# Kernel tuning notes

Hardware: AMD Instinct MI355X
Metric: run time of the kernel (lower is better)

The kernel has to match this reference:

```python
import jax, jax.numpy as jnp
import numpy as np

MAX_ACF_LAG = 6
TOP_K_FFT = 3
CLIP_VALUE = 5.0
EPS = 1e-8


def setup_inputs() -> dict:
    key = jax.random.key(0)
    x = jax.random.normal(key, (128, 4096, 32), dtype=jnp.float32)
    return {"x": x}


def _per_var_features(x):
    # x: [B, T, V] -> [B, V, 10 + MAX_ACF_LAG]
    B, T, V = x.shape
    mean = jnp.mean(x, axis=1)                      # [B, V]
    xc = x - mean[:, None, :]                       # centered, [B, T, V]
    var = jnp.mean(xc * xc, axis=1)                 # [B, V]
    std = jnp.sqrt(var + EPS)
    z = xc / std[:, None, :]
    skew = jnp.mean(z ** 3, axis=1)
    kurt = jnp.mean(z ** 4, axis=1)
    mn = jnp.min(x, axis=1)
    mx = jnp.max(x, axis=1)
    # linear trend slope via least squares on t = 0..T-1
    t = jnp.arange(T, dtype=x.dtype)
    tc = t - jnp.mean(t)
    slope = jnp.einsum('btv,t->bv', xc, tc) / jnp.sum(tc * tc)
    # top-k FFT magnitudes (exclude DC), normalized by T
    mag = jnp.abs(jnp.fft.rfft(x, axis=1))[:, 1:, :] / T   # [B, F, V]
    topk, _ = jax.lax.top_k(jnp.transpose(mag, (0, 2, 1)), TOP_K_FFT)  # [B, V, k]
    # autocorrelation at lags 1..MAX_ACF_LAG
    denom = jnp.sum(xc * xc, axis=1) + EPS          # [B, V]
    acfs = [jnp.sum(xc[:, :-lag, :] * xc[:, lag:, :], axis=1) / denom
            for lag in range(1, MAX_ACF_LAG + 1)]
    acf = jnp.stack(acfs, axis=-1)                  # [B, V, L]
    base = jnp.stack([mean, std, skew, kurt, mn, mx, slope], axis=-1)  # [B, V, 7]
    return jnp.concatenate([base, topk, acf], axis=-1)  # [B, V, 16]


def reference(x):
    feats = _per_var_features(x)                    # [B, V, 16]
    f_mean = jnp.mean(feats, axis=1)                # [B, 16]
    f_std = jnp.std(feats, axis=1)                  # [B, 16]
    out = jnp.concatenate([f_mean, f_std], axis=-1) # [B, 32]
    return jnp.clip(out, -CLIP_VALUE, CLIP_VALUE)
```

## Files before the change

### kernel.cpp

```cpp
#include <hip/hip_runtime.h>
#include <math.h>

#define T_LEN 4096
#define M_LEN 2048
#define V_DIM 32
#define B_DIM 128
#define NTHREADS 512
#define NWAVES (NTHREADS / 64)

__device__ __forceinline__ int SW(int i) { return i ^ (((i >> 4) & 7) << 1); }

__device__ __forceinline__ int fpos(int k) {
    return ((k & 3) << 9) | (((k >> 2) & 3) << 7) | (((k >> 4) & 3) << 5)
         | (((k >> 6) & 3) << 3) | (((k >> 8) & 3) << 1) | ((k >> 10) & 1);
}

__device__ __forceinline__ void ins3(float& a0, float& a1, float& a2, float m) {
    if (m > a0) { a2 = a1; a1 = a0; a0 = m; }
    else if (m > a1) { a2 = a1; a1 = m; }
    else if (m > a2) { a2 = m; }
}

template <typename Op>
__device__ __forceinline__ void block_reduce2(float& a, float& b, float* scr, Op op) {
    #pragma unroll
    for (int o = 32; o > 0; o >>= 1) {
        a = op(a, __shfl_down(a, o));
        b = op(b, __shfl_down(b, o));
    }
    int lane = threadIdx.x & 63, w = threadIdx.x >> 6;
    if (lane == 0) { scr[w * 2] = a; scr[w * 2 + 1] = b; }
    __syncthreads();
    if (threadIdx.x == 0) {
        float ra = scr[0], rb = scr[1];
        #pragma unroll
        for (int i = 1; i < NWAVES; i++) { ra = op(ra, scr[i * 2]); rb = op(rb, scr[i * 2 + 1]); }
        scr[2 * NWAVES] = ra; scr[2 * NWAVES + 1] = rb;
    }
    __syncthreads();
    a = scr[2 * NWAVES]; b = scr[2 * NWAVES + 1];
    __syncthreads();
}

__device__ __forceinline__ void block_reduce_sum10(float* v, float* scr) {
    #pragma unroll
    for (int r = 0; r < 10; r++) {
        #pragma unroll
        for (int o = 32; o > 0; o >>= 1) v[r] += __shfl_down(v[r], o);
    }
    int lane = threadIdx.x & 63, w = threadIdx.x >> 6;
    if (lane == 0) {
        #pragma unroll
        for (int r = 0; r < 10; r++) scr[w * 10 + r] = v[r];
    }
    __syncthreads();
    if (threadIdx.x < 10) {
        float s = 0.f;
        #pragma unroll
        for (int i = 0; i < NWAVES; i++) s += scr[i * 10 + threadIdx.x];
        scr[NWAVES * 10 + threadIdx.x] = s;
    }
    __syncthreads();
    #pragma unroll
    for (int r = 0; r < 10; r++) v[r] = scr[NWAVES * 10 + r];
    __syncthreads();
}

__global__ __launch_bounds__(NTHREADS, 8)
void ts_feat_kernel(const float* __restrict__ x, float* __restrict__ feats) {
    __shared__ __align__(16) float data[2][T_LEN];
    __shared__ float scr[128];
    float* const fd = &data[0][0];
    float2* const Z = reinterpret_cast<float2*>(fd);

    const int tid = threadIdx.x;
    const int bid  = blockIdx.x;
    const int xcd  = bid & 7;
    const int idx  = bid >> 3;
    const int b    = xcd + ((idx >> 4) << 3);
    const int pair = idx & 15;
    const int v0   = pair * 2;
    const int sid0 = b * V_DIM + v0;

    const float2* __restrict__ p2 =
        reinterpret_cast<const float2*>(x + (size_t)b * T_LEN * V_DIM + v0);

    float s0 = 0.f, s1 = 0.f;
    float mn0 = 3.4e38f, mn1 = 3.4e38f, mx0 = -3.4e38f, mx1 = -3.4e38f;
    const int comp = tid & 1;
    #pragma unroll
    for (int i = 0; i < T_LEN / NTHREADS; i++) {
        int t = tid + i * NTHREADS;
        float2 val = p2[(size_t)t * (V_DIM / 2)];
        int f = SW(t >> 1);
        fd[(f << 1) + comp] = val.x;
        fd[T_LEN + (f << 1) + comp] = val.y;
        s0 += val.x; s1 += val.y;
        mn0 = fminf(mn0, val.x); mn1 = fminf(mn1, val.y);
        mx0 = fmaxf(mx0, val.x); mx1 = fmaxf(mx1, val.y);
    }
    __syncthreads();
    block_reduce2(s0, s1, scr, [](float a, float c) { return a + c; });
    block_reduce2(mn0, mn1, scr, [](float a, float c) { return fminf(a, c); });
    block_reduce2(mx0, mx1, scr, [](float a, float c) { return fmaxf(a, c); });

    const float mean0 = s0 * (1.f / T_LEN);
    const float mean1 = s1 * (1.f / T_LEN);

    #pragma unroll 1
    for (int si = 0; si < 2; si++) {
        const float m = si ? mean1 : mean0;
        const int fb = (si << 11) + (tid << 2);
        float4 q0 = *reinterpret_cast<const float4*>(&Z[SW(fb)]);
        float4 q1 = *reinterpret_cast<const float4*>(&Z[SW(fb + 2)]);
        float4 q2 = make_float4(0.f, 0.f, 0.f, 0.f);
        float2 q3 = make_float2(0.f, 0.f);
        const bool interior = (tid < NTHREADS - 1);
        if (interior) {
            q2 = *reinterpret_cast<const float4*>(&Z[SW(fb + 4)]);
            q3 = Z[SW(fb + 6)];
        }
        float xc[8] = {q0.x - m, q0.y - m, q0.z - m, q0.w - m,
                       q1.x - m, q1.y - m, q1.z - m, q1.w - m};
        float xb[6];
        if (interior) {
            xb[0] = q2.x - m; xb[1] = q2.y - m; xb[2] = q2.z - m;
            xb[3] = q2.w - m; xb[4] = q3.x - m; xb[5] = q3.y - m;
        } else {
            #pragma unroll
            for (int u = 0; u < 6; u++) xb[u] = 0.f;
        }
        float acc[10];
        #pragma unroll
        for (int r = 0; r < 10; r++) acc[r] = 0.f;
        const float tf0 = (float)(tid * 8) - 2047.5f;
        #pragma unroll
        for (int u = 0; u < 8; u++) {
            float c = xc[u], c2v = c * c;
            acc[0] += c2v;
            acc[1] += c2v * c;
            acc[2] += c2v * c2v;
            acc[3] += c * (tf0 + (float)u);
        }
        #pragma unroll
        for (int L = 1; L <= 6; L++) {
            #pragma unroll
            for (int u = 0; u < 8; u++) {
                float nx = (u + L < 8) ? xc[u + L] : xb[u + L - 8];
                acc[3 + L] += xc[u] * nx;
            }
        }
        block_reduce_sum10(acc, scr);

        if (tid == 0) {
            const float c2 = acc[0], c3 = acc[1], c4 = acc[2], ct = acc[3];
            float var = c2 * (1.f / T_LEN);
            float sd  = sqrtf(var + 1e-8f);
            float i3  = 1.f / (sd * sd * sd);
            float skew = c3 * (1.f / T_LEN) * i3;
            float kurt = c4 * (1.f / T_LEN) * i3 / sd;
            float slope = ct / 5726622720.f;
            float dn = c2 + 1e-8f;
            float* fp = feats + (size_t)(sid0 + si) * 16;
            fp[0] = m; fp[1] = sd; fp[2] = skew; fp[3] = kurt;
            fp[4] = si ? mn1 : mn0;
            fp[5] = si ? mx1 : mx0;
            fp[6] = slope;
            fp[10] = acc[4] / dn;
            fp[11] = acc[5] / dn;
            fp[12] = acc[6] / dn;
            fp[13] = acc[7] / dn;
            fp[14] = acc[8] / dn;
            fp[15] = acc[9] / dn;
        }
    }

    #pragma unroll
    for (int st = 0; st < 5; st++) {
        const int lq = 9 - 2 * st;
        const int q  = 1 << lq;
        const float scale = -3.06796158e-3f * (float)(1 << (2 * st));
        __syncthreads();
        #pragma unroll
        for (int si = 0; si < 2; si++) {
            const int w = tid;
            const int g = w >> lq;
            const int j = w & (q - 1);
            const int base = (si << 11) + (g << (lq + 2)) + j;
            const int p0 = SW(base), p1 = SW(base + q);
            const int p2i = SW(base + 2 * q), p3 = SW(base + 3 * q);
            float2 a = Z[p0], bb = Z[p1], c = Z[p2i], d = Z[p3];
            float t0r = a.x + c.x,  t0i = a.y + c.y;
            float t1r = a.x - c.x,  t1i = a.y - c.y;
            float t2r = bb.x + d.x, t2i = bb.y + d.y;
            float t3r = bb.x - d.x, t3i = bb.y - d.y;
            float sn, cs;
            __sincosf(scale * (float)j, &sn, &cs);
            float c2 = cs * cs - sn * sn, s2 = 2.f * cs * sn;
            float c3 = c2 * cs - s2 * sn, s3 = c2 * sn + s2 * cs;
            float y1r = t1r + t3i, y1i = t1i - t3r;
            float y2r = t0r - t2r, y2i = t0i - t2i;
            float y3r = t1r - t3i, y3i = t1i + t3r;
            Z[p0]  = make_float2(t0r + t2r, t0i + t2i);
            Z[p1]  = make_float2(y1r * cs - y1i * sn, y1r * sn + y1i * cs);
            Z[p2i] = make_float2(y2r * c2 - y2i * s2, y2r * s2 + y2i * c2);
            Z[p3]  = make_float2(y3r * c3 - y3i * s3, y3r * s3 + y3i * c3);
        }
    }
    __syncthreads();
    #pragma unroll
    for (int bfI = 0; bfI < 4; bfI++) {
        int mI = tid + (bfI << 9);
        int si = mI >> 10, g = mI & 1023;
        int p = SW((si << 11) + (g << 1));
        float4 ab = *reinterpret_cast<float4*>(&Z[p]);
        float4 o;
        o.x = ab.x + ab.z; o.y = ab.y + ab.w;
        o.z = ab.x - ab.z; o.w = ab.y - ab.w;
        *reinterpret_cast<float4*>(&Z[p]) = o;
    }
    __syncthreads();

    const float inv_T = 1.f / (float)T_LEN;
    #pragma unroll 1
    for (int si = 0; si < 2; si++) {
        const int zb = si << 11;
        float a0 = -1.f, a1 = -1.f, a2 = -1.f;
        #pragma unroll
        for (int i = 0; i < M_LEN / NTHREADS; i++) {
            int k  = 1 + tid + i * NTHREADS;
            int ka = k & (M_LEN - 1);
            int kb = (M_LEN - k) & (M_LEN - 1);
            float2 Za = Z[zb + SW(fpos(ka))];
            float2 Zb = Z[zb + SW(fpos(kb))];
            float Er = 0.5f * (Za.x + Zb.x);
            float Ei = 0.5f * (Za.y - Zb.y);
            float Or = 0.5f * (Za.y + Zb.y);
            float Oi = 0.5f * (Zb.x - Za.x);
            float ang = (float)k * (-3.14159265358979f / (float)M_LEN);
            float sn, cs; __sincosf(ang, &sn, &cs);
            float Xr = Er + cs * Or - sn * Oi;
            float Xi = Ei + cs * Oi + sn * Or;
            float mag = sqrtf(Xr * Xr + Xi * Xi);
            ins3(a0, a1, a2, mag);
        }
        #pragma unroll
        for (int o = 32; o > 0; o >>= 1) {
            float b0 = __shfl_down(a0, o), b1 = __shfl_down(a1, o), b2 = __shfl_down(a2, o);
            ins3(a0, a1, a2, b0); ins3(a0, a1, a2, b1); ins3(a0, a1, a2, b2);
        }
        int lane = tid & 63, w = tid >> 6;
        if (lane == 0) { scr[w * 3 + 0] = a0; scr[w * 3 + 1] = a1; scr[w * 3 + 2] = a2; }
        __syncthreads();
        if (tid == 0) {
            float t0 = scr[0], t1 = scr[1], t2 = scr[2];
            #pragma unroll
            for (int w2 = 1; w2 < NWAVES; w2++) {
                ins3(t0, t1, t2, scr[w2 * 3 + 0]);
                ins3(t0, t1, t2, scr[w2 * 3 + 1]);
                ins3(t0, t1, t2, scr[w2 * 3 + 2]);
            }
            float* fp = feats + (size_t)(sid0 + si) * 16;
            fp[7] = t0 * inv_T; fp[8] = t1 * inv_T; fp[9] = t2 * inv_T;
        }
        __syncthreads();
    }
}

__global__ void ts_reduce_kernel(const float* __restrict__ feats, float* __restrict__ out) {
    int tg = blockIdx.x * blockDim.x + threadIdx.x;
    if (tg >= B_DIM * 16) return;
    int b = tg >> 4, f = tg & 15;
    const float* fp = feats + (size_t)b * V_DIM * 16 + f;
    float vals[V_DIM];
    float s = 0.f;
    #pragma unroll
    for (int v = 0; v < V_DIM; v++) { vals[v] = fp[v * 16]; s += vals[v]; }
    float m = s * (1.f / V_DIM);
    float q = 0.f;
    #pragma unroll
    for (int v = 0; v < V_DIM; v++) { float d = vals[v] - m; q += d * d; }
    float sd = sqrtf(q * (1.f / V_DIM));
    out[(size_t)b * 32 + f]      = fminf(fmaxf(m,  -5.f), 5.f);
    out[(size_t)b * 32 + 16 + f] = fminf(fmaxf(sd, -5.f), 5.f);
}

extern "C" void kernel_launch(void* const* d_in, const int* in_sizes, int n_in,
                              void* d_out, int out_size, void* d_ws, size_t ws_size,
                              hipStream_t stream) {
    const float* x = (const float*)d_in[0];
    float* out = (float*)d_out;
    float* feats = (float*)d_ws;

    hipLaunchKernelGGL(ts_feat_kernel, dim3(B_DIM * V_DIM / 2), dim3(NTHREADS), 0, stream,
                       x, feats);
    hipLaunchKernelGGL(ts_reduce_kernel, dim3(8), dim3(256), 0, stream,
                       feats, out);
}
```

Baseline: 155.0 us.

## Cut block barriers by merging reductions and overlapping stats with FFT stages

The three separate block reductions (sum, min, max) are merged into one pass with a single pair of barriers. The per-series 10-value moment/ACF reduction now writes partials for both series at once and finishes in the shadow of the first FFT stage, and feature finalisation overlaps the second stage. The final radix-2 pass is folded into the post-processing reads, and the top-3 search handles both series in one loop. The ACF now uses a sliding window over preceding elements rather than following ones. All of this removes many __syncthreads and one LDS round trip, at the cost of more shared scratch and registers.

```diff
diff --git a/kernel.cpp b/kernel.cpp
--- a/kernel.cpp
+++ b/kernel.cpp
@@ -6,7 +6,7 @@
 #define V_DIM 32
 #define B_DIM 128
 #define NTHREADS 512
-#define NWAVES (NTHREADS / 64)
+#define NWAVES 8
 
 __device__ __forceinline__ int SW(int i) { return i ^ (((i >> 4) & 7) << 1); }
 
@@ -21,55 +21,55 @@
     else if (m > a2) { a2 = m; }
 }
 
-template <typename Op>
-__device__ __forceinline__ void block_reduce2(float& a, float& b, float* scr, Op op) {
-    #pragma unroll
-    for (int o = 32; o > 0; o >>= 1) {
-        a = op(a, __shfl_down(a, o));
-        b = op(b, __shfl_down(b, o));
-    }
-    int lane = threadIdx.x & 63, w = threadIdx.x >> 6;
-    if (lane == 0) { scr[w * 2] = a; scr[w * 2 + 1] = b; }
-    __syncthreads();
-    if (threadIdx.x == 0) {
-        float ra = scr[0], rb = scr[1];
-        #pragma unroll
-        for (int i = 1; i < NWAVES; i++) { ra = op(ra, scr[i * 2]); rb = op(rb, scr[i * 2 + 1]); }
-        scr[2 * NWAVES] = ra; scr[2 * NWAVES + 1] = rb;
-    }
-    __syncthreads();
-    a = scr[2 * NWAVES]; b = scr[2 * NWAVES + 1];
-    __syncthreads();
-}
-
-__device__ __forceinline__ void block_reduce_sum10(float* v, float* scr) {
-    #pragma unroll
-    for (int r = 0; r < 10; r++) {
-        #pragma unroll
-        for (int o = 32; o > 0; o >>= 1) v[r] += __shfl_down(v[r], o);
-    }
-    int lane = threadIdx.x & 63, w = threadIdx.x >> 6;
-    if (lane == 0) {
-        #pragma unroll
-        for (int r = 0; r < 10; r++) scr[w * 10 + r] = v[r];
-    }
-    __syncthreads();
-    if (threadIdx.x < 10) {
-        float s = 0.f;
-        #pragma unroll
-        for (int i = 0; i < NWAVES; i++) s += scr[i * 10 + threadIdx.x];
-        scr[NWAVES * 10 + threadIdx.x] = s;
-    }
-    __syncthreads();
-    #pragma unroll
-    for (int r = 0; r < 10; r++) v[r] = scr[NWAVES * 10 + r];
-    __syncthreads();
+#define SCR_A_PART 0
+#define SCR_A_FIN  48
+#define SCR_B_PART 64
+#define SCR_B_FIN  704
+#define SCR_C_PART 724
+#define SCR_SIZE   772
+
+template <int ST>
+__device__ __forceinline__ void fft_stage(float2* Z, int tid) {
+    constexpr int lq = 9 - 2 * ST;
+    constexpr int q  = 1 << lq;
+    const float scale = -3.06796158e-3f * (float)(1 << (2 * ST));
+    #pragma unroll
+    for (int si = 0; si < 2; si++) {
+        const int g = tid >> lq;
+        const int j = tid & (q - 1);
+        const int base = (si << 11) + (g << (lq + 2)) + j;
+        const int p0 = SW(base), p1 = SW(base + q);
+        const int p2i = SW(base + 2 * q), p3 = SW(base + 3 * q);
+        float2 a = Z[p0], bb = Z[p1], c = Z[p2i], d = Z[p3];
+        float t0r = a.x + c.x,  t0i = a.y + c.y;
+        float t1r = a.x - c.x,  t1i = a.y - c.y;
+        float t2r = bb.x + d.x, t2i = bb.y + d.y;
+        float t3r = bb.x - d.x, t3i = bb.y - d.y;
+        float sn, cs;
+        __sincosf(scale * (float)j, &sn, &cs);
+        float c2 = cs * cs - sn * sn, s2 = 2.f * cs * sn;
+        float c3 = c2 * cs - s2 * sn, s3 = c2 * sn + s2 * cs;
+        float y1r = t1r + t3i, y1i = t1i - t3r;
+        float y2r = t0r - t2r, y2i = t0i - t2i;
+        float y3r = t1r - t3i, y3i = t1i + t3r;
+        Z[p0]  = make_float2(t0r + t2r, t0i + t2i);
+        Z[p1]  = make_float2(y1r * cs - y1i * sn, y1r * sn + y1i * cs);
+        Z[p2i] = make_float2(y2r * c2 - y2i * s2, y2r * s2 + y2i * c2);
+        Z[p3]  = make_float2(y3r * c3 - y3i * s3, y3r * s3 + y3i * c3);
+    }
+}
+
+__device__ __forceinline__ float2 rdpost(const float2* Z, int zb, int p) {
+    int e = p & ~1;
+    float4 v = *reinterpret_cast<const float4*>(&Z[zb + SW(e)]);
+    return (p & 1) ? make_float2(v.x - v.z, v.y - v.w)
+                   : make_float2(v.x + v.z, v.y + v.w);
 }
 
 __global__ __launch_bounds__(NTHREADS, 8)
 void ts_feat_kernel(const float* __restrict__ x, float* __restrict__ feats) {
     __shared__ __align__(16) float data[2][T_LEN];
-    __shared__ float scr[128];
+    __shared__ float scr[SCR_SIZE];
     float* const fd = &data[0][0];
     float2* const Z = reinterpret_cast<float2*>(fd);
 
@@ -89,7 +89,7 @@
     float mn0 = 3.4e38f, mn1 = 3.4e38f, mx0 = -3.4e38f, mx1 = -3.4e38f;
     const int comp = tid & 1;
     #pragma unroll
-    for (int i = 0; i < T_LEN / NTHREADS; i++) {
+    for (int i = 0; i < 8; i++) {
         int t = tid + i * NTHREADS;
         float2 val = p2[(size_t)t * (V_DIM / 2)];
         int f = SW(t >> 1);
@@ -99,13 +99,32 @@
         mn0 = fminf(mn0, val.x); mn1 = fminf(mn1, val.y);
         mx0 = fmaxf(mx0, val.x); mx1 = fmaxf(mx1, val.y);
     }
-    __syncthreads();
-    block_reduce2(s0, s1, scr, [](float a, float c) { return a + c; });
-    block_reduce2(mn0, mn1, scr, [](float a, float c) { return fminf(a, c); });
-    block_reduce2(mx0, mx1, scr, [](float a, float c) { return fmaxf(a, c); });
-
-    const float mean0 = s0 * (1.f / T_LEN);
-    const float mean1 = s1 * (1.f / T_LEN);
+    #pragma unroll
+    for (int o = 32; o > 0; o >>= 1) {
+        s0 += __shfl_down(s0, o); s1 += __shfl_down(s1, o);
+        mn0 = fminf(mn0, __shfl_down(mn0, o)); mn1 = fminf(mn1, __shfl_down(mn1, o));
+        mx0 = fmaxf(mx0, __shfl_down(mx0, o)); mx1 = fmaxf(mx1, __shfl_down(mx1, o));
+    }
+    const int lane = tid & 63, wv = tid >> 6;
+    if (lane == 0) {
+        float* p = &scr[SCR_A_PART + wv * 6];
+        p[0] = s0; p[1] = s1; p[2] = mn0; p[3] = mn1; p[4] = mx0; p[5] = mx1;
+    }
+    __syncthreads();
+    if (tid < 6) {
+        float r = scr[SCR_A_PART + tid];
+        #pragma unroll
+        for (int w = 1; w < NWAVES; w++) {
+            float v = scr[SCR_A_PART + w * 6 + tid];
+            r = (tid < 2) ? (r + v) : ((tid < 4) ? fminf(r, v) : fmaxf(r, v));
+        }
+        scr[SCR_A_FIN + tid] = r;
+    }
+    __syncthreads();
+    const float mean0 = scr[SCR_A_FIN + 0] * (1.f / T_LEN);
+    const float mean1 = scr[SCR_A_FIN + 1] * (1.f / T_LEN);
+    float fmn = 0.f, fmx = 0.f;
+    if (tid < 2) { fmn = scr[SCR_A_FIN + 2 + tid]; fmx = scr[SCR_A_FIN + 4 + tid]; }
 
     #pragma unroll 1
     for (int si = 0; si < 2; si++) {
@@ -113,157 +132,137 @@
         const int fb = (si << 11) + (tid << 2);
         float4 q0 = *reinterpret_cast<const float4*>(&Z[SW(fb)]);
         float4 q1 = *reinterpret_cast<const float4*>(&Z[SW(fb + 2)]);
-        float4 q2 = make_float4(0.f, 0.f, 0.f, 0.f);
-        float2 q3 = make_float2(0.f, 0.f);
-        const bool interior = (tid < NTHREADS - 1);
-        if (interior) {
-            q2 = *reinterpret_cast<const float4*>(&Z[SW(fb + 4)]);
-            q3 = Z[SW(fb + 6)];
-        }
-        float xc[8] = {q0.x - m, q0.y - m, q0.z - m, q0.w - m,
-                       q1.x - m, q1.y - m, q1.z - m, q1.w - m};
-        float xb[6];
-        if (interior) {
-            xb[0] = q2.x - m; xb[1] = q2.y - m; xb[2] = q2.z - m;
-            xb[3] = q2.w - m; xb[4] = q3.x - m; xb[5] = q3.y - m;
-        } else {
-            #pragma unroll
-            for (int u = 0; u < 6; u++) xb[u] = 0.f;
+        float p1v = 0.f, p2v = 0.f, p3v = 0.f, p4v = 0.f, p5v = 0.f, p6v = 0.f;
+        if (tid > 0) {
+            float2 tv = Z[SW(fb - 3)];
+            float4 tq = *reinterpret_cast<const float4*>(&Z[SW(fb - 2)]);
+            p6v = tv.x - m; p5v = tv.y - m;
+            p4v = tq.x - m; p3v = tq.y - m; p2v = tq.z - m; p1v = tq.w - m;
         }
         float acc[10];
         #pragma unroll
         for (int r = 0; r < 10; r++) acc[r] = 0.f;
         const float tf0 = (float)(tid * 8) - 2047.5f;
+        float xs[8] = {q0.x, q0.y, q0.z, q0.w, q1.x, q1.y, q1.z, q1.w};
         #pragma unroll
         for (int u = 0; u < 8; u++) {
-            float c = xc[u], c2v = c * c;
+            float c = xs[u] - m;
+            float c2v = c * c;
             acc[0] += c2v;
             acc[1] += c2v * c;
             acc[2] += c2v * c2v;
             acc[3] += c * (tf0 + (float)u);
-        }
-        #pragma unroll
-        for (int L = 1; L <= 6; L++) {
+            acc[4] += p1v * c; acc[5] += p2v * c; acc[6] += p3v * c;
+            acc[7] += p4v * c; acc[8] += p5v * c; acc[9] += p6v * c;
+            p6v = p5v; p5v = p4v; p4v = p3v; p3v = p2v; p2v = p1v; p1v = c;
+        }
+        #pragma unroll
+        for (int r = 0; r < 10; r++) {
+            acc[r] += __shfl_down(acc[r], 32);
+            acc[r] += __shfl_down(acc[r], 16);
+            acc[r] += __shfl_down(acc[r], 8);
+            acc[r] += __shfl_down(acc[r], 4);
+        }
+        if (lane < 4) {
             #pragma unroll
-            for (int u = 0; u < 8; u++) {
-                float nx = (u + L < 8) ? xc[u + L] : xb[u + L - 8];
-                acc[3 + L] += xc[u] * nx;
-            }
-        }
-        block_reduce_sum10(acc, scr);
-
-        if (tid == 0) {
-            const float c2 = acc[0], c3 = acc[1], c4 = acc[2], ct = acc[3];
-            float var = c2 * (1.f / T_LEN);
-            float sd  = sqrtf(var + 1e-8f);
-            float i3  = 1.f / (sd * sd * sd);
-            float skew = c3 * (1.f / T_LEN) * i3;
-            float kurt = c4 * (1.f / T_LEN) * i3 / sd;
-            float slope = ct / 5726622720.f;
-            float dn = c2 + 1e-8f;
-            float* fp = feats + (size_t)(sid0 + si) * 16;
-            fp[0] = m; fp[1] = sd; fp[2] = skew; fp[3] = kurt;
-            fp[4] = si ? mn1 : mn0;
-            fp[5] = si ? mx1 : mx0;
-            fp[6] = slope;
-            fp[10] = acc[4] / dn;
-            fp[11] = acc[5] / dn;
-            fp[12] = acc[6] / dn;
-            fp[13] = acc[7] / dn;
-            fp[14] = acc[8] / dn;
-            fp[15] = acc[9] / dn;
-        }
-    }
-
-    #pragma unroll
-    for (int st = 0; st < 5; st++) {
-        const int lq = 9 - 2 * st;
-        const int q  = 1 << lq;
-        const float scale = -3.06796158e-3f * (float)(1 << (2 * st));
-        __syncthreads();
-        #pragma unroll
-        for (int si = 0; si < 2; si++) {
-            const int w = tid;
-            const int g = w >> lq;
-            const int j = w & (q - 1);
-            const int base = (si << 11) + (g << (lq + 2)) + j;
-            const int p0 = SW(base), p1 = SW(base + q);
-            const int p2i = SW(base + 2 * q), p3 = SW(base + 3 * q);
-            float2 a = Z[p0], bb = Z[p1], c = Z[p2i], d = Z[p3];
-            float t0r = a.x + c.x,  t0i = a.y + c.y;
-            float t1r = a.x - c.x,  t1i = a.y - c.y;
-            float t2r = bb.x + d.x, t2i = bb.y + d.y;
-            float t3r = bb.x - d.x, t3i = bb.y - d.y;
-            float sn, cs;
-            __sincosf(scale * (float)j, &sn, &cs);
-            float c2 = cs * cs - sn * sn, s2 = 2.f * cs * sn;
-            float c3 = c2 * cs - s2 * sn, s3 = c2 * sn + s2 * cs;
-            float y1r = t1r + t3i, y1i = t1i - t3r;
-            float y2r = t0r - t2r, y2i = t0i - t2i;
-            float y3r = t1r - t3i, y3i = t1i + t3r;
-            Z[p0]  = make_float2(t0r + t2r, t0i + t2i);
-            Z[p1]  = make_float2(y1r * cs - y1i * sn, y1r * sn + y1i * cs);
-            Z[p2i] = make_float2(y2r * c2 - y2i * s2, y2r * s2 + y2i * c2);
-            Z[p3]  = make_float2(y3r * c3 - y3i * s3, y3r * s3 + y3i * c3);
-        }
-    }
-    __syncthreads();
-    #pragma unroll
-    for (int bfI = 0; bfI < 4; bfI++) {
-        int mI = tid + (bfI << 9);
-        int si = mI >> 10, g = mI & 1023;
-        int p = SW((si << 11) + (g << 1));
-        float4 ab = *reinterpret_cast<float4*>(&Z[p]);
-        float4 o;
-        o.x = ab.x + ab.z; o.y = ab.y + ab.w;
-        o.z = ab.x - ab.z; o.w = ab.y - ab.w;
-        *reinterpret_cast<float4*>(&Z[p]) = o;
-    }
+            for (int r = 0; r < 10; r++)
+                scr[SCR_B_PART + si * 320 + wv * 40 + lane * 10 + r] = acc[r];
+        }
+    }
+    __syncthreads();
+
+    if (tid < 10) {
+        float s = 0.f;
+        #pragma unroll
+        for (int e = 0; e < 32; e++) s += scr[SCR_B_PART + e * 10 + tid];
+        scr[SCR_B_FIN + tid] = s;
+    } else if (tid >= 16 && tid < 26) {
+        const int f = tid - 16;
+        float s = 0.f;
+        #pragma unroll
+        for (int e = 0; e < 32; e++) s += scr[SCR_B_PART + 320 + e * 10 + f];
+        scr[SCR_B_FIN + 10 + f] = s;
+    }
+    fft_stage<0>(Z, tid);
+    __syncthreads();
+
+    if (tid < 2) {
+        const float* A = &scr[SCR_B_FIN + tid * 10];
+        const float m = tid ? mean1 : mean0;
+        float c2 = A[0], c3 = A[1], c4 = A[2], ct = A[3];
+        float var = c2 * (1.f / T_LEN);
+        float sd  = sqrtf(var + 1e-8f);
+        float i3  = 1.f / (sd * sd * sd);
+        float dn  = c2 + 1e-8f;
+        float* fp = feats + (size_t)(sid0 + tid) * 16;
+        fp[0] = m; fp[1] = sd;
+        fp[2] = c3 * (1.f / T_LEN) * i3;
+        fp[3] = c4 * (1.f / T_LEN) * i3 / sd;
+        fp[4] = fmn; fp[5] = fmx;
+        fp[6] = ct / 5726622720.f;
+        fp[10] = A[4] / dn; fp[11] = A[5] / dn; fp[12] = A[6] / dn;
+        fp[13] = A[7] / dn; fp[14] = A[8] / dn; fp[15] = A[9] / dn;
+    }
+    fft_stage<1>(Z, tid);
+    __syncthreads();
+    fft_stage<2>(Z, tid);
+    __syncthreads();
+    fft_stage<3>(Z, tid);
+    __syncthreads();
+    fft_stage<4>(Z, tid);
     __syncthreads();
 
     const float inv_T = 1.f / (float)T_LEN;
-    #pragma unroll 1
-    for (int si = 0; si < 2; si++) {
-        const int zb = si << 11;
-        float a0 = -1.f, a1 = -1.f, a2 = -1.f;
-        #pragma unroll
-        for (int i = 0; i < M_LEN / NTHREADS; i++) {
-            int k  = 1 + tid + i * NTHREADS;
-            int ka = k & (M_LEN - 1);
-            int kb = (M_LEN - k) & (M_LEN - 1);
-            float2 Za = Z[zb + SW(fpos(ka))];
-            float2 Zb = Z[zb + SW(fpos(kb))];
-            float Er = 0.5f * (Za.x + Zb.x);
-            float Ei = 0.5f * (Za.y - Zb.y);
-            float Or = 0.5f * (Za.y + Zb.y);
-            float Oi = 0.5f * (Zb.x - Za.x);
-            float ang = (float)k * (-3.14159265358979f / (float)M_LEN);
-            float sn, cs; __sincosf(ang, &sn, &cs);
+    float a0 = -1.f, a1 = -1.f, a2 = -1.f;
+    float b0 = -1.f, b1 = -1.f, b2 = -1.f;
+    #pragma unroll
+    for (int i = 0; i < 4; i++) {
+        int k  = 1 + tid + i * NTHREADS;
+        int ka = k & (M_LEN - 1);
+        int kb = (M_LEN - k) & (M_LEN - 1);
+        int pa = fpos(ka), pb = fpos(kb);
+        float ang = (float)k * (-3.14159265358979f / (float)M_LEN);
+        float sn, cs; __sincosf(ang, &sn, &cs);
+        {
+            float2 Za = rdpost(Z, 0, pa), Zb = rdpost(Z, 0, pb);
+            float Er = 0.5f * (Za.x + Zb.x), Ei = 0.5f * (Za.y - Zb.y);
+            float Or = 0.5f * (Za.y + Zb.y), Oi = 0.5f * (Zb.x - Za.x);
             float Xr = Er + cs * Or - sn * Oi;
             float Xi = Ei + cs * Oi + sn * Or;
-            float mag = sqrtf(Xr * Xr + Xi * Xi);
-            ins3(a0, a1, a2, mag);
-        }
-        #pragma unroll
-        for (int o = 32; o > 0; o >>= 1) {
-            float b0 = __shfl_down(a0, o), b1 = __shfl_down(a1, o), b2 = __shfl_down(a2, o);
-            ins3(a0, a1, a2, b0); ins3(a0, a1, a2, b1); ins3(a0, a1, a2, b2);
-        }
-        int lane = tid & 63, w = tid >> 6;
-        if (lane == 0) { scr[w * 3 + 0] = a0; scr[w * 3 + 1] = a1; scr[w * 3 + 2] = a2; }
-        __syncthreads();
-        if (tid == 0) {
-            float t0 = scr[0], t1 = scr[1], t2 = scr[2];
-            #pragma unroll
-            for (int w2 = 1; w2 < NWAVES; w2++) {
-                ins3(t0, t1, t2, scr[w2 * 3 + 0]);
-                ins3(t0, t1, t2, scr[w2 * 3 + 1]);
-                ins3(t0, t1, t2, scr[w2 * 3 + 2]);
-            }
-            float* fp = feats + (size_t)(sid0 + si) * 16;
-            fp[7] = t0 * inv_T; fp[8] = t1 * inv_T; fp[9] = t2 * inv_T;
-        }
-        __syncthreads();
+            ins3(a0, a1, a2, sqrtf(Xr * Xr + Xi * Xi));
+        }
+        {
+            float2 Za = rdpost(Z, M_LEN, pa), Zb = rdpost(Z, M_LEN, pb);
+            float Er = 0.5f * (Za.x + Zb.x), Ei = 0.5f * (Za.y - Zb.y);
+            float Or = 0.5f * (Za.y + Zb.y), Oi = 0.5f * (Zb.x - Za.x);
+            float Xr = Er + cs * Or - sn * Oi;
+            float Xi = Ei + cs * Oi + sn * Or;
+            ins3(b0, b1, b2, sqrtf(Xr * Xr + Xi * Xi));
+        }
+    }
+    #pragma unroll
+    for (int o = 32; o > 0; o >>= 1) {
+        float u0 = __shfl_down(a0, o), u1 = __shfl_down(a1, o), u2 = __shfl_down(a2, o);
+        ins3(a0, a1, a2, u0); ins3(a0, a1, a2, u1); ins3(a0, a1, a2, u2);
+        float w0 = __shfl_down(b0, o), w1 = __shfl_down(b1, o), w2 = __shfl_down(b2, o);
+        ins3(b0, b1, b2, w0); ins3(b0, b1, b2, w1); ins3(b0, b1, b2, w2);
+    }
+    if (lane == 0) {
+        float* p = &scr[SCR_C_PART + wv * 6];
+        p[0] = a0; p[1] = a1; p[2] = a2; p[3] = b0; p[4] = b1; p[5] = b2;
+    }
+    __syncthreads();
+    if (tid < 2) {
+        const int off = SCR_C_PART + tid * 3;
+        float t0 = scr[off], t1 = scr[off + 1], t2 = scr[off + 2];
+        #pragma unroll
+        for (int w = 1; w < NWAVES; w++) {
+            ins3(t0, t1, t2, scr[off + w * 6]);
+            ins3(t0, t1, t2, scr[off + w * 6 + 1]);
+            ins3(t0, t1, t2, scr[off + w * 6 + 2]);
+        }
+        float* fp = feats + (size_t)(sid0 + tid) * 16;
+        fp[7] = t0 * inv_T; fp[8] = t1 * inv_T; fp[9] = t2 * inv_T;
     }
 }
 
```

After: 147.2 us. 1.05x faster.
